# Kernel optimization log

Hardware: AMD Instinct MI355X
Metric: run time of the kernel (lower is better)

The kernel has to match this reference:

```python
import jax, jax.numpy as jnp
import numpy as np

NUM_GROUP = 512
GROUP_SIZE = 32


def setup_inputs() -> dict:
    key = jax.random.key(0)
    pts = jax.random.normal(key, (8, 8192, 6), dtype=jnp.float32)
    return {"pts": pts}


def _fps(xyz, num_group):
    """Farthest point sampling. xyz: (B, N, 3) -> indices (B, G)."""
    B, N, _ = xyz.shape

    def body(carry, _):
        dist, far = carry  # dist: (B, N) running min sq-dist to chosen set; far: (B,)
        centroid = jnp.take_along_axis(xyz, far[:, None, None], axis=1)  # (B, 1, 3)
        d = jnp.sum((xyz - centroid) ** 2, axis=-1)  # (B, N)
        dist = jnp.minimum(dist, d)
        new_far = jnp.argmax(dist, axis=-1)  # (B,)
        return (dist, new_far), far

    init = (jnp.full((B, N), 1e10, dtype=xyz.dtype), jnp.zeros((B,), dtype=jnp.int32))
    _, idxs = jax.lax.scan(body, init, None, length=num_group)  # (G, B)
    return idxs.T  # (B, G)


def _knn(k, xyz, center):
    """k nearest neighbors of each center among xyz. Returns idx (B, G, k)."""
    # squared distances (B, G, N)
    d2 = (jnp.sum(center ** 2, -1)[:, :, None]
          + jnp.sum(xyz ** 2, -1)[:, None, :]
          - 2.0 * jnp.einsum('bgc,bnc->bgn', center, xyz))
    _, idx = jax.lax.top_k(-d2, k)
    return idx


def reference(pts):
    xyz = pts[:, :, :3].astype(jnp.float32)
    fps_idx = _fps(xyz, NUM_GROUP)  # (B, G)
    center = jnp.take_along_axis(xyz, fps_idx[:, :, None], axis=1)  # (B, G, 3)
    idx = _knn(GROUP_SIZE, xyz, center)  # (B, G, K)
    # gather neighborhoods per batch: pts (B, N, C), idx (B, G, K) -> (B, G, K, C)
    neighborhood = jax.vmap(lambda p, i: p[i])(pts, idx)
    # center only the xyz channels
    nb_xyz = neighborhood[..., :3] - center[:, :, None, :]
    neighborhood = jnp.concatenate([nb_xyz, neighborhood[..., 3:]], axis=-1)
    return (neighborhood, center)
```

## Files before the change

kernel.cpp:

```cpp
#include <hip/hip_runtime.h>
#include <stdint.h>

#define BATCH 8
#define NPTS 8192
#define NGRP 512
#define KNN 32
#define NCH 6

#define FPS_T 256
#define FPS_PPT (NPTS / FPS_T)

__global__ __launch_bounds__(FPS_T) void fps_kernel(const float* __restrict__ pts,
                                                    float* __restrict__ out_ctr) {
    __shared__ float xs[NPTS], ys[NPTS], zs[NPTS];
    __shared__ unsigned long long slots[2][FPS_T / 64];

    const int b   = blockIdx.x;
    const int tid = threadIdx.x;
    const float* base = pts + (size_t)b * NPTS * NCH;

    float x[FPS_PPT], y[FPS_PPT], z[FPS_PPT], dist[FPS_PPT];
#pragma unroll
    for (int j = 0; j < FPS_PPT; ++j) {
        int p = tid + j * FPS_T;
        x[j] = base[p * NCH + 0];
        y[j] = base[p * NCH + 1];
        z[j] = base[p * NCH + 2];
        xs[p] = x[j]; ys[p] = y[j]; zs[p] = z[j];
        dist[j] = 1e10f;
    }
    __syncthreads();

    int far = 0;
    float* ctr = out_ctr + (size_t)b * NGRP * 3;

    for (int g = 0; g < NGRP; ++g) {
        float cx = xs[far], cy = ys[far], cz = zs[far];
        if (tid == 0) {
            ctr[g * 3 + 0] = cx;
            ctr[g * 3 + 1] = cy;
            ctr[g * 3 + 2] = cz;
        }

        float bestv = -1.0f;
        int bestj = 0;
#pragma unroll
        for (int j = 0; j < FPS_PPT; ++j) {
            float dx = __fsub_rn(x[j], cx);
            float dy = __fsub_rn(y[j], cy);
            float dz = __fsub_rn(z[j], cz);
            float d = __fadd_rn(__fadd_rn(__fmul_rn(dx, dx), __fmul_rn(dy, dy)),
                                __fmul_rn(dz, dz));
            float nd = fminf(dist[j], d);
            dist[j] = nd;
            if (nd > bestv) { bestv = nd; bestj = j; }
        }
        int bestp = tid + bestj * FPS_T;
        unsigned long long key =
            ((unsigned long long)__float_as_uint(bestv) << 13) |
            (unsigned)(8191 - bestp);

#pragma unroll
        for (int s = 32; s > 0; s >>= 1) {
            unsigned long long o = __shfl_xor(key, s, 64);
            key = (o > key) ? o : key;
        }
        int wid = tid >> 6;
        if ((tid & 63) == 0) slots[g & 1][wid] = key;
        __syncthreads();

        unsigned long long best = slots[g & 1][0];
#pragma unroll
        for (int w = 1; w < FPS_T / 64; ++w) {
            unsigned long long o = slots[g & 1][w];
            best = (o > best) ? o : best;
        }
        far = 8191 - (int)(best & 8191ULL);
    }
}

__device__ __forceinline__ unsigned long long knn_key(const float* __restrict__ base,
                                                      int p, float cx, float cy,
                                                      float cz, float cc) {
    float x = base[p * NCH + 0];
    float y = base[p * NCH + 1];
    float z = base[p * NCH + 2];
    float xx = __fadd_rn(__fadd_rn(__fmul_rn(x, x), __fmul_rn(y, y)), __fmul_rn(z, z));
    float dt = fmaf(cz, z, fmaf(cy, y, __fmul_rn(cx, x)));
    float d2 = __fsub_rn(__fadd_rn(cc, xx), __fmul_rn(2.0f, dt));
    unsigned int bits = __float_as_uint(d2);
    unsigned int ord = bits ^ ((unsigned)((int)bits >> 31) | 0x80000000u);
    return ((unsigned long long)ord << 13) | (unsigned)p;
}

__global__ __launch_bounds__(64) void knn_kernel(const float* __restrict__ pts,
                                                 const float* __restrict__ ctr,
                                                 float* __restrict__ out_nb) {
    const int bg   = blockIdx.x;
    const int b    = bg >> 9;
    const int lane = threadIdx.x & 63;
    const float* base = pts + (size_t)b * NPTS * NCH;

    const float cx = ctr[bg * 3 + 0];
    const float cy = ctr[bg * 3 + 1];
    const float cz = ctr[bg * 3 + 2];
    const float cc = __fadd_rn(__fadd_rn(__fmul_rn(cx, cx), __fmul_rn(cy, cy)),
                               __fmul_rn(cz, cz));

    unsigned long long R = knn_key(base, lane, cx, cy, cz, cc);
#pragma unroll
    for (int k = 2; k <= 64; k <<= 1) {
#pragma unroll
        for (int j = k >> 1; j > 0; j >>= 1) {
            unsigned long long o = __shfl_xor(R, j, 64);
            bool takeMin = (((lane & k) == 0) == ((lane & j) == 0));
            unsigned long long mn = (o < R) ? o : R;
            unsigned long long mx = (o < R) ? R : o;
            R = takeMin ? mn : mx;
        }
    }
    unsigned long long R31 = __shfl(R, 31, 64);

    for (int c = 1; c < NPTS / 64; ++c) {
        unsigned long long key = knn_key(base, c * 64 + lane, cx, cy, cz, cc);
        unsigned long long qual = __ballot(key < R31);
        while (qual) {
            int src = __ffsll(qual) - 1;
            qual &= qual - 1;
            unsigned long long bk = __shfl(key, src, 64);
            int rank = __popcll(__ballot(R < bk));
            unsigned long long Rp = __shfl_up(R, 1, 64);
            R = (lane == rank) ? bk : ((lane > rank) ? Rp : R);
            R31 = __shfl(R, 31, 64);
        }
    }

    if (lane < KNN) {
        int idx = (int)(R & 8191ULL);
        const float* s = base + (size_t)idx * NCH;
        float* d = out_nb + ((size_t)bg * KNN + lane) * NCH;
        d[0] = s[0] - cx;
        d[1] = s[1] - cy;
        d[2] = s[2] - cz;
        d[3] = s[3];
        d[4] = s[4];
        d[5] = s[5];
    }
}

extern "C" void kernel_launch(void* const* d_in, const int* in_sizes, int n_in,
                              void* d_out, int out_size, void* d_ws, size_t ws_size,
                              hipStream_t stream) {
    const float* pts = (const float*)d_in[0];
    float* out = (float*)d_out;
    float* out_nb  = out;
    float* out_ctr = out + (size_t)BATCH * NGRP * KNN * NCH;

    hipLaunchKernelGGL(fps_kernel, dim3(BATCH), dim3(FPS_T), 0, stream, pts, out_ctr);
    hipLaunchKernelGGL(knn_kernel, dim3(BATCH * NGRP), dim3(64), 0, stream,
                       pts, out_ctr, out_nb);
}
```

Baseline: 591.8 us.

## Widen FPS block and use precomputed SoA coordinates for KNN scan

Raises the FPS kernel from 256 to 1024 threads, so each thread holds 8 points instead of 32 and the serial per-iteration work shrinks, at the cost of a 16-wave reduction per step. Adds a pre-pass that writes x, y, z and squared norms into workspace as structure-of-arrays, so the KNN scan reads coalesced floats instead of strided 24-byte records and skips recomputing the norm. The SoA path only runs when the workspace is large enough, and the extra kernel adds launch and memory traffic.

```diff
diff --git a/kernel.cpp b/kernel.cpp
--- a/kernel.cpp
+++ b/kernel.cpp
@@ -7,13 +7,14 @@
 #define KNN 32
 #define NCH 6
 
-#define FPS_T 256
+#define FPS_T 1024
 #define FPS_PPT (NPTS / FPS_T)
+#define FPS_NW (FPS_T / 64)
 
 __global__ __launch_bounds__(FPS_T) void fps_kernel(const float* __restrict__ pts,
                                                     float* __restrict__ out_ctr) {
     __shared__ float xs[NPTS], ys[NPTS], zs[NPTS];
-    __shared__ unsigned long long slots[2][FPS_T / 64];
+    __shared__ unsigned long long slots[2][FPS_NW];
 
     const int b   = blockIdx.x;
     const int tid = threadIdx.x;
@@ -71,7 +72,7 @@
 
         unsigned long long best = slots[g & 1][0];
 #pragma unroll
-        for (int w = 1; w < FPS_T / 64; ++w) {
+        for (int w = 1; w < FPS_NW; ++w) {
             unsigned long long o = slots[g & 1][w];
             best = (o > best) ? o : best;
         }
@@ -79,27 +80,61 @@
     }
 }
 
-__device__ __forceinline__ unsigned long long knn_key(const float* __restrict__ base,
-                                                      int p, float cx, float cy,
-                                                      float cz, float cc) {
+__global__ __launch_bounds__(256) void soa_kernel(const float* __restrict__ pts,
+                                                  float* __restrict__ xs,
+                                                  float* __restrict__ ys,
+                                                  float* __restrict__ zs,
+                                                  float* __restrict__ xx) {
+    int i = blockIdx.x * blockDim.x + threadIdx.x;
+    const float* s = pts + (size_t)i * NCH;
+    float x = s[0], y = s[1], z = s[2];
+    xs[i] = x; ys[i] = y; zs[i] = z;
+    xx[i] = __fadd_rn(__fadd_rn(__fmul_rn(x, x), __fmul_rn(y, y)), __fmul_rn(z, z));
+}
+
+__device__ __forceinline__ unsigned long long pack_key(float d2, int p) {
+    unsigned int bits = __float_as_uint(d2);
+    unsigned int ord = bits ^ ((unsigned)((int)bits >> 31) | 0x80000000u);
+    return ((unsigned long long)ord << 13) | (unsigned)p;
+}
+
+__device__ __forceinline__ unsigned long long knn_key_aos(const float* __restrict__ base,
+                                                          int p, float cx, float cy,
+                                                          float cz, float cc) {
     float x = base[p * NCH + 0];
     float y = base[p * NCH + 1];
     float z = base[p * NCH + 2];
     float xx = __fadd_rn(__fadd_rn(__fmul_rn(x, x), __fmul_rn(y, y)), __fmul_rn(z, z));
     float dt = fmaf(cz, z, fmaf(cy, y, __fmul_rn(cx, x)));
     float d2 = __fsub_rn(__fadd_rn(cc, xx), __fmul_rn(2.0f, dt));
-    unsigned int bits = __float_as_uint(d2);
-    unsigned int ord = bits ^ ((unsigned)((int)bits >> 31) | 0x80000000u);
-    return ((unsigned long long)ord << 13) | (unsigned)p;
-}
-
+    return pack_key(d2, p);
+}
+
+__device__ __forceinline__ unsigned long long knn_key_soa(const float* __restrict__ xs,
+                                                          const float* __restrict__ ys,
+                                                          const float* __restrict__ zs,
+                                                          const float* __restrict__ xx,
+                                                          int i, int p, float cx,
+                                                          float cy, float cz, float cc) {
+    float x = xs[i], y = ys[i], z = zs[i], q = xx[i];
+    float dt = fmaf(cz, z, fmaf(cy, y, __fmul_rn(cx, x)));
+    float d2 = __fsub_rn(__fadd_rn(cc, q), __fmul_rn(2.0f, dt));
+    return pack_key(d2, p);
+}
+
+template <int SOA>
 __global__ __launch_bounds__(64) void knn_kernel(const float* __restrict__ pts,
                                                  const float* __restrict__ ctr,
-                                                 float* __restrict__ out_nb) {
+                                                 float* __restrict__ out_nb,
+                                                 const float* __restrict__ xs,
+                                                 const float* __restrict__ ys,
+                                                 const float* __restrict__ zs,
+                                                 const float* __restrict__ xx) {
     const int bg   = blockIdx.x;
     const int b    = bg >> 9;
     const int lane = threadIdx.x & 63;
     const float* base = pts + (size_t)b * NPTS * NCH;
+    const int ibase = b * NPTS;
 
     const float cx = ctr[bg * 3 + 0];
     const float cy = ctr[bg * 3 + 1];
@@ -107,7 +142,9 @@
     const float cc = __fadd_rn(__fadd_rn(__fmul_rn(cx, cx), __fmul_rn(cy, cy)),
                                __fmul_rn(cz, cz));
 
-    unsigned long long R = knn_key(base, lane, cx, cy, cz, cc);
+    unsigned long long R = SOA
+        ? knn_key_soa(xs, ys, zs, xx, ibase + lane, lane, cx, cy, cz, cc)
+        : knn_key_aos(base, lane, cx, cy, cz, cc);
 #pragma unroll
     for (int k = 2; k <= 64; k <<= 1) {
 #pragma unroll
@@ -122,7 +159,10 @@
     unsigned long long R31 = __shfl(R, 31, 64);
 
     for (int c = 1; c < NPTS / 64; ++c) {
-        unsigned long long key = knn_key(base, c * 64 + lane, cx, cy, cz, cc);
+        int p = c * 64 + lane;
+        unsigned long long key = SOA
+            ? knn_key_soa(xs, ys, zs, xx, ibase + p, p, cx, cy, cz, cc)
+            : knn_key_aos(base, p, cx, cy, cz, cc);
         unsigned long long qual = __ballot(key < R31);
         while (qual) {
             int src = __ffsll(qual) - 1;
@@ -156,7 +196,23 @@
     float* out_nb  = out;
     float* out_ctr = out + (size_t)BATCH * NGRP * KNN * NCH;
 
+    const size_t npts_tot = (size_t)BATCH * NPTS;
+    float* xs = (float*)d_ws;
+    float* ys = xs + npts_tot;
+    float* zs = ys + npts_tot;
+    float* xx = zs + npts_tot;
+    bool use_soa = ws_size >= 4 * npts_tot * sizeof(float);
+
+    if (use_soa) {
+        hipLaunchKernelGGL(soa_kernel, dim3(npts_tot / 256), dim3(256), 0, stream,
+                           pts, xs, ys, zs, xx);
+    }
     hipLaunchKernelGGL(fps_kernel, dim3(BATCH), dim3(FPS_T), 0, stream, pts, out_ctr);
-    hipLaunchKernelGGL(knn_kernel, dim3(BATCH * NGRP), dim3(64), 0, stream,
-                       pts, out_ctr, out_nb);
-}
+    if (use_soa) {
+        hipLaunchKernelGGL((knn_kernel<1>), dim3(BATCH * NGRP), dim3(64), 0, stream,
+                           pts, out_ctr, out_nb, xs, ys, zs, xx);
+    } else {
+        hipLaunchKernelGGL((knn_kernel<0>), dim3(BATCH * NGRP), dim3(64), 0, stream,
+                           pts, out_ctr, out_nb, xs, ys, zs, xx);
+    }
+}
```

Measured after the change: 746.3 us. 26.1% more time.

## Speed up FPS argmax with packed math, DPP max reduction and atomicMin index

Applied to the files above, without the earlier changes.

Doubles the FPS block to 512 threads and computes squared distances in pairs with v_pk_add/v_pk_mul. The argmax no longer reduces 64-bit value/index keys through shuffles. Instead it reduces only the float max with DPP row operations and a small LDS slot array, and the owning threads then post their smallest matching index with atomicMin. Centroids are staged in LDS and written to global memory once at the end. The aim is to shorten the serial 512-step loop, at the cost of a second barrier per iteration and a per-thread rescan of registers when a thread holds the max.

```diff
diff --git a/kernel.cpp b/kernel.cpp
--- a/kernel.cpp
+++ b/kernel.cpp
@@ -7,76 +7,121 @@
 #define KNN 32
 #define NCH 6
 
-#define FPS_T 256
+#define FPS_T 512
 #define FPS_PPT (NPTS / FPS_T)
+#define PAIRS (FPS_PPT / 2)
+#define FPS_NW (FPS_T / 64)
+
+typedef float f2 __attribute__((ext_vector_type(2)));
+
+__device__ __forceinline__ f2 pk_add(f2 a, f2 b) {
+    f2 d;
+    asm("v_pk_add_f32 %0, %1, %2" : "=v"(d) : "v"(a), "v"(b));
+    return d;
+}
+__device__ __forceinline__ f2 pk_mul(f2 a, f2 b) {
+    f2 d;
+    asm("v_pk_mul_f32 %0, %1, %2" : "=v"(d) : "v"(a), "v"(b));
+    return d;
+}
+
+template <int CTRL>
+__device__ __forceinline__ float dpp_fmax(float v) {
+    int s = __builtin_amdgcn_update_dpp(__float_as_int(v), __float_as_int(v),
+                                        CTRL, 0xF, 0xF, false);
+    return fmaxf(v, __int_as_float(s));
+}
 
 __global__ __launch_bounds__(FPS_T) void fps_kernel(const float* __restrict__ pts,
                                                     float* __restrict__ out_ctr) {
     __shared__ float xs[NPTS], ys[NPTS], zs[NPTS];
-    __shared__ unsigned long long slots[2][FPS_T / 64];
+    __shared__ float ctr_lds[NGRP * 3];
+    __shared__ float wslot[FPS_NW];
+    __shared__ unsigned int islot[2];
 
     const int b   = blockIdx.x;
     const int tid = threadIdx.x;
     const float* base = pts + (size_t)b * NPTS * NCH;
 
-    float x[FPS_PPT], y[FPS_PPT], z[FPS_PPT], dist[FPS_PPT];
-#pragma unroll
-    for (int j = 0; j < FPS_PPT; ++j) {
-        int p = tid + j * FPS_T;
-        x[j] = base[p * NCH + 0];
-        y[j] = base[p * NCH + 1];
-        z[j] = base[p * NCH + 2];
-        xs[p] = x[j]; ys[p] = y[j]; zs[p] = z[j];
-        dist[j] = 1e10f;
+    f2 x2[PAIRS], y2[PAIRS], z2[PAIRS], dist2[PAIRS];
+#pragma unroll
+    for (int i = 0; i < PAIRS; ++i) {
+        int p0 = tid + (2 * i) * FPS_T;
+        int p1 = tid + (2 * i + 1) * FPS_T;
+        float xa = base[p0 * NCH + 0], ya = base[p0 * NCH + 1], za = base[p0 * NCH + 2];
+        float xb = base[p1 * NCH + 0], yb = base[p1 * NCH + 1], zb = base[p1 * NCH + 2];
+        x2[i] = (f2){xa, xb};
+        y2[i] = (f2){ya, yb};
+        z2[i] = (f2){za, zb};
+        dist2[i] = (f2){1e10f, 1e10f};
+        xs[p0] = xa; ys[p0] = ya; zs[p0] = za;
+        xs[p1] = xb; ys[p1] = yb; zs[p1] = zb;
     }
     __syncthreads();
 
     int far = 0;
-    float* ctr = out_ctr + (size_t)b * NGRP * 3;
+    const int wid  = tid >> 6;
+    const int lane = tid & 63;
 
     for (int g = 0; g < NGRP; ++g) {
         float cx = xs[far], cy = ys[far], cz = zs[far];
         if (tid == 0) {
-            ctr[g * 3 + 0] = cx;
-            ctr[g * 3 + 1] = cy;
-            ctr[g * 3 + 2] = cz;
-        }
+            ctr_lds[g * 3 + 0] = cx;
+            ctr_lds[g * 3 + 1] = cy;
+            ctr_lds[g * 3 + 2] = cz;
+            islot[g & 1] = 0xFFFFFFFFu;
+        }
+        f2 ncx = (f2){-cx, -cx};
+        f2 ncy = (f2){-cy, -cy};
+        f2 ncz = (f2){-cz, -cz};
 
         float bestv = -1.0f;
-        int bestj = 0;
-#pragma unroll
-        for (int j = 0; j < FPS_PPT; ++j) {
-            float dx = __fsub_rn(x[j], cx);
-            float dy = __fsub_rn(y[j], cy);
-            float dz = __fsub_rn(z[j], cz);
-            float d = __fadd_rn(__fadd_rn(__fmul_rn(dx, dx), __fmul_rn(dy, dy)),
-                                __fmul_rn(dz, dz));
-            float nd = fminf(dist[j], d);
-            dist[j] = nd;
-            if (nd > bestv) { bestv = nd; bestj = j; }
-        }
-        int bestp = tid + bestj * FPS_T;
-        unsigned long long key =
-            ((unsigned long long)__float_as_uint(bestv) << 13) |
-            (unsigned)(8191 - bestp);
-
-#pragma unroll
-        for (int s = 32; s > 0; s >>= 1) {
-            unsigned long long o = __shfl_xor(key, s, 64);
-            key = (o > key) ? o : key;
-        }
-        int wid = tid >> 6;
-        if ((tid & 63) == 0) slots[g & 1][wid] = key;
+#pragma unroll
+        for (int i = 0; i < PAIRS; ++i) {
+            f2 dx = pk_add(x2[i], ncx);
+            f2 dy = pk_add(y2[i], ncy);
+            f2 dz = pk_add(z2[i], ncz);
+            f2 sx = pk_mul(dx, dx);
+            f2 sy = pk_mul(dy, dy);
+            f2 t  = pk_add(sx, sy);
+            f2 sz = pk_mul(dz, dz);
+            f2 d  = pk_add(t, sz);
+            float nd0 = fminf(dist2[i].x, d.x);
+            float nd1 = fminf(dist2[i].y, d.y);
+            dist2[i].x = nd0;
+            dist2[i].y = nd1;
+            bestv = fmaxf(fmaxf(nd0, nd1), bestv);
+        }
+
+        float m = bestv;
+        m = dpp_fmax<0x111>(m);
+        m = dpp_fmax<0x112>(m);
+        m = dpp_fmax<0x114>(m);
+        m = dpp_fmax<0x118>(m);
+        m = dpp_fmax<0x142>(m);
+        m = dpp_fmax<0x143>(m);
+        if (lane == 63) wslot[wid] = m;
         __syncthreads();
 
-        unsigned long long best = slots[g & 1][0];
-#pragma unroll
-        for (int w = 1; w < FPS_T / 64; ++w) {
-            unsigned long long o = slots[g & 1][w];
-            best = (o > best) ? o : best;
-        }
-        far = 8191 - (int)(best & 8191ULL);
-    }
+        float M = wslot[0];
+#pragma unroll
+        for (int w = 1; w < FPS_NW; ++w) M = fmaxf(M, wslot[w]);
+
+        if (bestv == M) {
+            int bj = 0;
+#pragma unroll
+            for (int i = PAIRS - 1; i >= 0; --i) {
+                if (dist2[i].y == M) bj = 2 * i + 1;
+                if (dist2[i].x == M) bj = 2 * i;
+            }
+            atomicMin(&islot[g & 1], (unsigned)(tid + bj * FPS_T));
+        }
+        __syncthreads();
+        far = (int)islot[g & 1];
+    }
+
+    float* ctr = out_ctr + (size_t)b * NGRP * 3;
+    for (int i = tid; i < NGRP * 3; i += FPS_T) ctr[i] = ctr_lds[i];
 }
 
 __device__ __forceinline__ unsigned long long knn_key(const float* __restrict__ base,
```

Measured after the change: 572.7 us. -3.2%, faster.
